# Kernel tuning notes

Measured on AMD Instinct MI355X. Metric: run time of the kernel, lower is better.

The kernel has to match this reference:

```python
import jax, jax.numpy as jnp
import numpy as np

KS = 3      # kernel size
PAD = 1     # zero padding
STRIDE = 1
N = KS * KS # 9 sampling points per pixel


def _deform_conv(feature, offset, weight):
    """DeformConv2d: bilinear sample at learned offsets then 3x3 conv (no bias)."""
    b, c, h, w = feature.shape
    x = jnp.pad(feature, ((0, 0), (0, 0), (PAD, PAD), (PAD, PAD)))
    hp, wp = h + 2 * PAD, w + 2 * PAD
    dt = feature.dtype
    # p_n: kernel grid offsets, x(rows) first then y(cols) -> (2N,)
    rng = jnp.arange(-(KS - 1) // 2, (KS - 1) // 2 + 1, dtype=dt)
    pn_x, pn_y = jnp.meshgrid(rng, rng, indexing='ij')
    # p_0: base sampling grid starting at 1 (accounts for zero padding)
    p0_x, p0_y = jnp.meshgrid(jnp.arange(1, h + 1, dtype=dt),
                              jnp.arange(1, w + 1, dtype=dt), indexing='ij')
    # sampling locations p = p_0 + p_n + offset, split into x/y -> (b,h,w,N)
    off = jnp.transpose(offset, (0, 2, 3, 1))  # (b,h,w,2N)
    px = p0_x[None, :, :, None] + pn_x.reshape(-1)[None, None, None, :] + off[..., :N]
    py = p0_y[None, :, :, None] + pn_y.reshape(-1)[None, None, None, :] + off[..., N:]
    q_lt_x = jnp.clip(jnp.floor(px), 0, hp - 1)
    q_lt_y = jnp.clip(jnp.floor(py), 0, wp - 1)
    q_rb_x = jnp.clip(jnp.floor(px) + 1, 0, hp - 1)
    q_rb_y = jnp.clip(jnp.floor(py) + 1, 0, wp - 1)
    px = jnp.clip(px, 0, hp - 1)
    py = jnp.clip(py, 0, wp - 1)
    # bilinear weights for the 4 corners
    g_lt = (1 + (q_lt_x - px)) * (1 + (q_lt_y - py))
    g_rb = (1 - (q_rb_x - px)) * (1 - (q_rb_y - py))
    g_lb = (1 + (q_lt_x - px)) * (1 - (q_rb_y - py))
    g_rt = (1 - (q_rb_x - px)) * (1 + (q_lt_y - py))
    x_flat = x.reshape(b, c, hp * wp)

    def gather(qx, qy):
        idx = (qx * wp + qy).astype(jnp.int32).reshape(b, 1, -1)
        v = jnp.take_along_axis(x_flat, jnp.broadcast_to(idx, (b, c, h * w * N)), axis=2)
        return v.reshape(b, c, h, w, N)

    x_off = (g_lt[:, None] * gather(q_lt_x, q_lt_y)
             + g_rb[:, None] * gather(q_rb_x, q_rb_y)
             + g_lb[:, None] * gather(q_lt_x, q_rb_y)
             + g_rt[:, None] * gather(q_rb_x, q_lt_y))  # (b,c,h,w,N)
    # equivalent of _reshape_x_offset + conv(ks, stride=ks)
    x_off = x_off.reshape(b, c, h, w, KS, KS)
    return jnp.einsum('bchwij,ocij->bohw', x_off, weight)


def setup_inputs() -> dict:
    key = jax.random.key(0)
    k1, k2, k3 = jax.random.split(key, 3)
    B, C, H, W = 4, 256, 64, 64
    feature = jax.random.normal(k1, (B, C, H, W), dtype=jnp.float32)
    offset = jax.random.normal(k2, (B, 2 * N, H, W), dtype=jnp.float32)
    weight = jax.random.normal(k3, (C, C, KS, KS), dtype=jnp.float32) / np.sqrt(C * N)
    return {"feature": feature, "offset": offset, "weight": weight}


def reference(feature, offset, weight):
    f1 = jax.nn.relu(_deform_conv(feature, offset, weight))
    return jax.nn.relu(f1 + feature)
```

## Files before the change

### kernel.cpp

```cpp
#include <hip/hip_runtime.h>

#define HW    4096
#define J_TOT 16384
#define K_TOT 2304
#define C_CH  256

typedef unsigned short u16;
typedef unsigned int   u32;
typedef __attribute__((ext_vector_type(8))) short short8;
typedef __attribute__((ext_vector_type(4))) float f32x4;
typedef __attribute__((ext_vector_type(4))) unsigned short us4;

__device__ __forceinline__ float b2f(u16 u) { return __uint_as_float(((u32)u) << 16); }
__device__ __forceinline__ u16 f2b(float x) {
  u32 u = __float_as_uint(x);
  u += 0x7FFFu + ((u >> 16) & 1u);
  return (u16)(u >> 16);
}

__device__ __forceinline__ void gload_lds16(const u16* g, u16* l) {
  __builtin_amdgcn_global_load_lds(
      (__attribute__((address_space(1))) void*)(void*)g,
      (__attribute__((address_space(3))) void*)(void*)l, 16, 0, 0);
}

__global__ void k_detect(const u16* __restrict__ f, int* __restrict__ flag) {
  __shared__ int sh[256];
  int t = threadIdx.x;
  int hits = 0;
  for (int i = t; i < 2048; i += 256) {
    u16 u = f[2 * i];
    int e = (u >> 7) & 0xFF;
    hits += (e >= 100 && e <= 141) ? 1 : 0;
  }
  sh[t] = hits;
  __syncthreads();
  if (t == 0) {
    int s = 0;
    for (int i = 0; i < 256; i++) s += sh[i];
    flag[0] = (s > 1024) ? 1 : 0;
  }
}

__global__ void k_prep(const void* __restrict__ featv, u16* __restrict__ ftr,
                       const void* __restrict__ wv, u16* __restrict__ Wr,
                       const int* __restrict__ flag) {
  int isbf = *flag;
  int tx = threadIdx.x;
  int ty = threadIdx.y;
  int z = blockIdx.z;
  if (z < 4) {
    __shared__ u16 tile[32][33];
    int b = z;
    int hw0 = blockIdx.x << 5;
    int c0 = blockIdx.y << 5;
    if (isbf) {
      const u16* f = (const u16*)featv;
#pragma unroll
      for (int i = 0; i < 4; i++) {
        int c = c0 + ty + i * 8;
        tile[ty + i * 8][tx] = f[(((size_t)(b * C_CH + c)) << 12) + hw0 + tx];
      }
    } else {
      const float* f = (const float*)featv;
#pragma unroll
      for (int i = 0; i < 4; i++) {
        int c = c0 + ty + i * 8;
        tile[ty + i * 8][tx] = f2b(f[(((size_t)(b * C_CH + c)) << 12) + hw0 + tx]);
      }
    }
    __syncthreads();
#pragma unroll
    for (int i = 0; i < 4; i++) {
      int hw = hw0 + ty + i * 8;
      ftr[(((size_t)(b * HW + hw)) << 8) + c0 + tx] = tile[tx][ty + i * 8];
    }
  } else {
    int bid = blockIdx.x + (blockIdx.y << 7);
    int flat = ty * 32 + tx;
    for (int idx = bid * 256 + flat; idx < C_CH * K_TOT; idx += 1024 * 256) {
      int c = idx & 255;
      int n = (idx >> 8) % 9;
      int o = idx / K_TOT;
      int src = (o * 256 + c) * 9 + n;
      if (isbf) Wr[idx] = ((const u16*)wv)[src];
      else      Wr[idx] = f2b(((const float*)wv)[src]);
    }
  }
}

#define NT 36

#define A_DMA(Ab)                                                            \
  do {                                                                       \
    gload_lds16(asrc0, (Ab) + wave * 1024);                                  \
    gload_lds16(asrc1, (Ab) + wave * 1024 + 512);                            \
    asrc0 += 64; asrc1 += 64;                                                \
  } while (0)

#define PLOAD_S(tile, P)                                                     \
  do {                                                                       \
    if (((tile) & 3) == 0) {                                                 \
      int np_ = (tile) >> 2;                                                 \
      tw0 = gs[np_][0][pp]; tw1 = gs[np_][1][pp];                            \
      tw2 = gs[np_][2][pp]; tw3 = gs[np_][3][pp];                            \
      ti0 = isx[np_][0][pp]; ti1 = isx[np_][1][pp];                          \
      ti2 = isx[np_][2][pp]; ti3 = isx[np_][3][pp];                          \
    }                                                                        \
    int c0_ = (((tile) & 3) << 6) + cb4;                                     \
    P##w0 = tw0; P##w1 = tw1; P##w2 = tw2; P##w3 = tw3;                      \
    P##q0 = *(const us4*)(ftr + ti0 + c0_);                                  \
    P##q1 = *(const us4*)(ftr + ti1 + c0_);                                  \
    P##q2 = *(const us4*)(ftr + ti2 + c0_);                                  \
    P##q3 = *(const us4*)(ftr + ti3 + c0_);                                  \
  } while (0)

#define PFIN_S(P, Bb)                                                        \
  do {                                                                       \
    us4 ov;                                                                  \
    _Pragma("unroll")                                                        \
    for (int i = 0; i < 4; i++) {                                            \
      float v = P##w0 * b2f(P##q0[i]) + P##w1 * b2f(P##q1[i]) +              \
                P##w2 * b2f(P##q2[i]) + P##w3 * b2f(P##q3[i]);               \
      ov[i] = f2b(v);                                                        \
    }                                                                        \
    *(us4*)((Bb) + bofs) = ov;                                               \
  } while (0)

#define GEMM_COMPUTE(Ab, Bb)                                                 \
  do {                                                                       \
    short8 af[2][2], bf[2][2];                                               \
    _Pragma("unroll")                                                        \
    for (int kk = 0; kk < 2; kk++) {                                         \
      int go = (((kk << 2) + lk) ^ swz) << 3;                                \
      _Pragma("unroll")                                                      \
      for (int oi = 0; oi < 2; oi++)                                         \
        af[oi][kk] = *(const short8*)((Ab) + (wo * 32 + oi * 16 + lr) * 64 + go); \
      _Pragma("unroll")                                                      \
      for (int ji = 0; ji < 2; ji++)                                         \
        bf[ji][kk] = *(const short8*)((Bb) + (wj * 32 + ji * 16 + lr) * 64 + go); \
    }                                                                        \
    __builtin_amdgcn_s_setprio(1);                                           \
    _Pragma("unroll")                                                        \
    for (int kk = 0; kk < 2; kk++)                                           \
      _Pragma("unroll")                                                      \
      for (int oi = 0; oi < 2; oi++)                                         \
        _Pragma("unroll")                                                    \
        for (int ji = 0; ji < 2; ji++)                                       \
          acc[oi][ji] = __builtin_amdgcn_mfma_f32_16x16x32_bf16(             \
              af[oi][kk], bf[ji][kk], acc[oi][ji], 0, 0, 0);                 \
    __builtin_amdgcn_s_setprio(0);                                           \
  } while (0)

#define CBAR()                                                               \
  do {                                                                       \
    asm volatile("s_waitcnt vmcnt(6) lgkmcnt(0)" ::: "memory");              \
    __builtin_amdgcn_s_barrier();                                            \
  } while (0)

#define ROTATE()                                                             \
  do {                                                                       \
    u16* tp_ = Ac; Ac = An; An = Af; Af = tp_;                               \
    tp_ = Bc; Bc = Bn; Bn = Bf; Bf = tp_;                                    \
  } while (0)

__global__ __launch_bounds__(1024, 4) void k_gemm(const u16* __restrict__ Wr,
                                                  const u16* __restrict__ ftr,
                                                  const void* __restrict__ offv,
                                                  const void* __restrict__ featv,
                                                  void* __restrict__ outv,
                                                  const int* __restrict__ flag) {
  __shared__ u16 As[3][256 * 64];
  __shared__ u16 Bs[3][64 * 64];
  __shared__ float gs[9][4][64];
  __shared__ int   isx[9][4][64];
  int isbf = *flag;
  asm volatile("" :: "s"(isbf));
  int j0 = blockIdx.x << 6;
  int b = j0 >> 12;
  int hw0 = j0 & (HW - 1);
  int t = threadIdx.x;
  int wave = t >> 6, lane = t & 63;
  int wj = wave >> 3, wo = wave & 7;
  int lr = lane & 15, lk = lane >> 4;
  int swz = lr & 7;

  if (t < 576) {
    int n = t >> 6, p = t & 63;
    int hw = hw0 + p;
    int h = hw >> 6, w = hw & 63;
    size_t obi = (((size_t)(b * 18 + n)) << 12) + hw;
    float ox, oy;
    if (isbf) {
      const u16* po = (const u16*)offv;
      ox = b2f(po[obi]);
      oy = b2f(po[obi + (9u << 12)]);
    } else {
      const float* po = (const float*)offv;
      ox = po[obi];
      oy = po[obi + (9u << 12)];
    }
    int ki = n / 3, kj = n % 3;
    float px = (float)(h + ki) + ox;
    float py = (float)(w + kj) + oy;
    float fx = floorf(px), fy = floorf(py);
    float qltx = fminf(fmaxf(fx, 0.f), 65.f);
    float qlty = fminf(fmaxf(fy, 0.f), 65.f);
    float qrbx = fminf(fmaxf(fx + 1.f, 0.f), 65.f);
    float qrby = fminf(fmaxf(fy + 1.f, 0.f), 65.f);
    float pcx = fminf(fmaxf(px, 0.f), 65.f);
    float pcy = fminf(fmaxf(py, 0.f), 65.f);
    float dltx = 1.f + (qltx - pcx);
    float drbx = 1.f - (qrbx - pcx);
    float dlty = 1.f + (qlty - pcy);
    float drby = 1.f - (qrby - pcy);
    float g0 = dltx * dlty;
    float g1 = drbx * drby;
    float g2 = dltx * drby;
    float g3 = drbx * dlty;
    int x0 = (int)qltx, y0 = (int)qlty, x1 = (int)qrbx, y1 = (int)qrby;
    int v0 = (x0 >= 1 && x0 <= 64 && y0 >= 1 && y0 <= 64);
    int v1 = (x1 >= 1 && x1 <= 64 && y1 >= 1 && y1 <= 64);
    int v2 = (x0 >= 1 && x0 <= 64 && y1 >= 1 && y1 <= 64);
    int v3 = (x1 >= 1 && x1 <= 64 && y0 >= 1 && y0 <= 64);
    int base = b << 12;
    isx[n][0][p] = v0 ? ((base + ((x0 - 1) << 6) + (y0 - 1)) << 8) : 0;
    isx[n][1][p] = v1 ? ((base + ((x1 - 1) << 6) + (y1 - 1)) << 8) : 0;
    isx[n][2][p] = v2 ? ((base + ((x0 - 1) << 6) + (y1 - 1)) << 8) : 0;
    isx[n][3][p] = v3 ? ((base + ((x1 - 1) << 6) + (y0 - 1)) << 8) : 0;
    gs[n][0][p] = v0 ? g0 : 0.f;
    gs[n][1][p] = v1 ? g1 : 0.f;
    gs[n][2][p] = v2 ? g2 : 0.f;
    gs[n][3][p] = v3 ? g3 : 0.f;
  }

  f32x4 acc[2][2];
  f32x4 zero = {0.f, 0.f, 0.f, 0.f};
#pragma unroll
  for (int i = 0; i < 2; i++)
#pragma unroll
    for (int j = 0; j < 2; j++) acc[i][j] = zero;

  int rb = lane >> 3;
  int cs = ((lane & 7) ^ rb) << 3;
  const u16* asrc0 = Wr + (size_t)(wave * 16 + 0 + rb) * K_TOT + cs;
  const u16* asrc1 = Wr + (size_t)(wave * 16 + 8 + rb) * K_TOT + cs;

  int pp = t >> 4, qq = t & 15;
  int cgp = qq >> 1, half = qq & 1;
  int bofs = pp * 64 + ((cgp ^ (pp & 7)) << 3) + (half << 2);
  int cb4 = (cgp << 3) + (half << 2);

  u16 *Ac = &As[0][0], *An = &As[1][0], *Af = &As[2][0];
  u16 *Bc = &Bs[0][0], *Bn = &Bs[1][0], *Bf = &Bs[2][0];

  __syncthreads();

  us4 aq0, aq1, aq2, aq3, bq0, bq1, bq2, bq3;
  float aw0, aw1, aw2, aw3, bw0, bw1, bw2, bw3;
  float tw0, tw1, tw2, tw3;
  int ti0, ti1, ti2, ti3;

  PLOAD_S(0, a); A_DMA(Ac);
  PFIN_S(a, Bc);
  PLOAD_S(1, b); A_DMA(An);
  CBAR();

#pragma unroll 1
  for (int it = 0; it < 17; ++it) {
    PLOAD_S(2 * it + 2, a);
    A_DMA(Af);
    GEMM_COMPUTE(Ac, Bc);
    PFIN_S(b, Bn);
    CBAR();
    ROTATE();
    PLOAD_S(2 * it + 3, b);
    A_DMA(Af);
    GEMM_COMPUTE(Ac, Bc);
    PFIN_S(a, Bn);
    CBAR();
    ROTATE();
  }
  GEMM_COMPUTE(Ac, Bc);
  PFIN_S(b, Bn);
  asm volatile("s_waitcnt vmcnt(0) lgkmcnt(0)" ::: "memory");
  __builtin_amdgcn_s_barrier();
  GEMM_COMPUTE(An, Bn);

  int lq = lane >> 4;
#pragma unroll
  for (int oi = 0; oi < 2; oi++) {
#pragma unroll
    for (int ji = 0; ji < 2; ji++) {
      int j = j0 + wj * 32 + ji * 16 + lr;
      int bb_ = j >> 12, hw = j & (HW - 1);
      int o0 = wo * 32 + oi * 16 + lq * 4;
#pragma unroll
      for (int r = 0; r < 4; r++) {
        size_t oidx = (((size_t)(bb_ * C_CH + o0 + r)) << 12) + hw;
        float v = acc[oi][ji][r];
        v = fmaxf(v, 0.f);
        float ft = isbf ? b2f(((const u16*)featv)[oidx]) : ((const float*)featv)[oidx];
        v = fmaxf(v + ft, 0.f);
        if (isbf) ((u16*)outv)[oidx] = f2b(v);
        else      ((float*)outv)[oidx] = v;
      }
    }
  }
}

extern "C" void kernel_launch(void* const* d_in, const int* in_sizes, int n_in,
                              void* d_out, int out_size, void* d_ws, size_t ws_size,
                              hipStream_t stream) {
  const void* feat = d_in[0];
  const void* offs = d_in[1];
  const void* wght = d_in[2];

  const size_t off_flag = 0;
  const size_t off_wr   = 256;
  const size_t off_ftr  = off_wr + (size_t)1179648;
  const size_t need     = off_ftr + (size_t)8388608;
  if (ws_size < need) return;

  char* ws = (char*)d_ws;
  int* flag = (int*)(ws + off_flag);
  u16* Wr   = (u16*)(ws + off_wr);
  u16* ftr  = (u16*)(ws + off_ftr);

  k_detect<<<1, 256, 0, stream>>>((const u16*)feat, flag);
  k_prep<<<dim3(128, 8, 5), dim3(32, 8), 0, stream>>>(feat, ftr, wght, Wr, flag);
  k_gemm<<<J_TOT / 64, 1024, 0, stream>>>(Wr, ftr, offs, feat, d_out, flag);
}
```

Before: 128.0 us.

## Load weight fragments directly to registers and halve GEMM block tile

Replaces the LDS-staged DMA of weight tiles with direct global-to-register loads of MFMA fragments, prefetched one K-step ahead. Blocks shrink to 512 threads covering 32 pixel columns, doubling the grid, and block IDs are remapped to spread neighbouring tiles across dies. This frees LDS and barrier pressure but doubles weight reads from L2 and relies on compiler-inserted waits for global latency.

```diff
diff --git a/kernel.cpp b/kernel.cpp
--- a/kernel.cpp
+++ b/kernel.cpp
@@ -16,12 +16,6 @@
   u32 u = __float_as_uint(x);
   u += 0x7FFFu + ((u >> 16) & 1u);
   return (u16)(u >> 16);
-}
-
-__device__ __forceinline__ void gload_lds16(const u16* g, u16* l) {
-  __builtin_amdgcn_global_load_lds(
-      (__attribute__((address_space(1))) void*)(void*)g,
-      (__attribute__((address_space(3))) void*)(void*)l, 16, 0, 0);
 }
 
 __global__ void k_detect(const u16* __restrict__ f, int* __restrict__ flag) {
@@ -91,11 +85,15 @@
 
 #define NT 36
 
-#define A_DMA(Ab)                                                            \
-  do {                                                                       \
-    gload_lds16(asrc0, (Ab) + wave * 1024);                                  \
-    gload_lds16(asrc1, (Ab) + wave * 1024 + 512);                            \
-    asrc0 += 64; asrc1 += 64;                                                \
+#define MFMA_ __builtin_amdgcn_mfma_f32_16x16x32_bf16
+
+#define ALOAD(tile, P)                                                       \
+  do {                                                                       \
+    const u16* ab_ = Wr + awoff + (tile) * 64;                               \
+    P##00 = *(const short8*)(ab_);                                           \
+    P##01 = *(const short8*)(ab_ + 32);                                      \
+    P##10 = *(const short8*)(ab_ + 16 * K_TOT);                              \
+    P##11 = *(const short8*)(ab_ + 16 * K_TOT + 32);                         \
   } while (0)
 
 #define PLOAD_S(tile, P)                                                     \
@@ -127,66 +125,60 @@
     *(us4*)((Bb) + bofs) = ov;                                               \
   } while (0)
 
-#define GEMM_COMPUTE(Ab, Bb)                                                 \
-  do {                                                                       \
-    short8 af[2][2], bf[2][2];                                               \
-    _Pragma("unroll")                                                        \
-    for (int kk = 0; kk < 2; kk++) {                                         \
-      int go = (((kk << 2) + lk) ^ swz) << 3;                                \
-      _Pragma("unroll")                                                      \
-      for (int oi = 0; oi < 2; oi++)                                         \
-        af[oi][kk] = *(const short8*)((Ab) + (wo * 32 + oi * 16 + lr) * 64 + go); \
-      _Pragma("unroll")                                                      \
-      for (int ji = 0; ji < 2; ji++)                                         \
-        bf[ji][kk] = *(const short8*)((Bb) + (wj * 32 + ji * 16 + lr) * 64 + go); \
-    }                                                                        \
+#define GEMM_COMPUTE(P, Bb)                                                  \
+  do {                                                                       \
+    int go0 = (lk ^ swz) << 3;                                               \
+    int go1 = ((4 + lk) ^ swz) << 3;                                         \
+    short8 b00 = *(const short8*)((Bb) + lr * 64 + go0);                     \
+    short8 b10 = *(const short8*)((Bb) + (16 + lr) * 64 + go0);              \
+    short8 b01 = *(const short8*)((Bb) + lr * 64 + go1);                     \
+    short8 b11 = *(const short8*)((Bb) + (16 + lr) * 64 + go1);              \
     __builtin_amdgcn_s_setprio(1);                                           \
-    _Pragma("unroll")                                                        \
-    for (int kk = 0; kk < 2; kk++)                                           \
-      _Pragma("unroll")                                                      \
-      for (int oi = 0; oi < 2; oi++)                                         \
-        _Pragma("unroll")                                                    \
-        for (int ji = 0; ji < 2; ji++)                                       \
-          acc[oi][ji] = __builtin_amdgcn_mfma_f32_16x16x32_bf16(             \
-              af[oi][kk], bf[ji][kk], acc[oi][ji], 0, 0, 0);                 \
+    acc[0][0] = MFMA_(P##00, b00, acc[0][0], 0, 0, 0);                       \
+    acc[0][1] = MFMA_(P##00, b10, acc[0][1], 0, 0, 0);                       \
+    acc[1][0] = MFMA_(P##10, b00, acc[1][0], 0, 0, 0);                       \
+    acc[1][1] = MFMA_(P##10, b10, acc[1][1], 0, 0, 0);                       \
+    acc[0][0] = MFMA_(P##01, b01, acc[0][0], 0, 0, 0);                       \
+    acc[0][1] = MFMA_(P##01, b11, acc[0][1], 0, 0, 0);                       \
+    acc[1][0] = MFMA_(P##11, b01, acc[1][0], 0, 0, 0);                       \
+    acc[1][1] = MFMA_(P##11, b11, acc[1][1], 0, 0, 0);                       \
     __builtin_amdgcn_s_setprio(0);                                           \
   } while (0)
 
 #define CBAR()                                                               \
   do {                                                                       \
-    asm volatile("s_waitcnt vmcnt(6) lgkmcnt(0)" ::: "memory");              \
+    asm volatile("s_waitcnt lgkmcnt(0)" ::: "memory");                       \
     __builtin_amdgcn_s_barrier();                                            \
   } while (0)
 
 #define ROTATE()                                                             \
   do {                                                                       \
-    u16* tp_ = Ac; Ac = An; An = Af; Af = tp_;                               \
-    tp_ = Bc; Bc = Bn; Bn = Bf; Bf = tp_;                                    \
-  } while (0)
-
-__global__ __launch_bounds__(1024, 4) void k_gemm(const u16* __restrict__ Wr,
-                                                  const u16* __restrict__ ftr,
-                                                  const void* __restrict__ offv,
-                                                  const void* __restrict__ featv,
-                                                  void* __restrict__ outv,
-                                                  const int* __restrict__ flag) {
-  __shared__ u16 As[3][256 * 64];
-  __shared__ u16 Bs[3][64 * 64];
-  __shared__ float gs[9][4][64];
-  __shared__ int   isx[9][4][64];
+    u16* tp_ = Bc; Bc = Bn; Bn = Bf; Bf = tp_;                               \
+  } while (0)
+
+__global__ __launch_bounds__(512, 4) void k_gemm(const u16* __restrict__ Wr,
+                                                 const u16* __restrict__ ftr,
+                                                 const void* __restrict__ offv,
+                                                 const void* __restrict__ featv,
+                                                 void* __restrict__ outv,
+                                                 const int* __restrict__ flag) {
+  __shared__ u16 Bs[3][32 * 64];
+  __shared__ float gs[9][4][32];
+  __shared__ int   isx[9][4][32];
   int isbf = *flag;
-  asm volatile("" :: "s"(isbf));
-  int j0 = blockIdx.x << 6;
+  int bid = blockIdx.x;
+  int xb = (bid & 7) * 64 + (bid >> 3);
+  int j0 = xb << 5;
   int b = j0 >> 12;
   int hw0 = j0 & (HW - 1);
   int t = threadIdx.x;
   int wave = t >> 6, lane = t & 63;
-  int wj = wave >> 3, wo = wave & 7;
+  int wo = wave;
   int lr = lane & 15, lk = lane >> 4;
   int swz = lr & 7;
 
-  if (t < 576) {
-    int n = t >> 6, p = t & 63;
+  if (t < 288) {
+    int n = t >> 5, p = t & 31;
     int hw = hw0 + p;
     int h = hw >> 6, w = hw & 63;
     size_t obi = (((size_t)(b * 18 + n)) << 12) + hw;
@@ -241,17 +233,13 @@
 #pragma unroll
     for (int j = 0; j < 2; j++) acc[i][j] = zero;
 
-  int rb = lane >> 3;
-  int cs = ((lane & 7) ^ rb) << 3;
-  const u16* asrc0 = Wr + (size_t)(wave * 16 + 0 + rb) * K_TOT + cs;
-  const u16* asrc1 = Wr + (size_t)(wave * 16 + 8 + rb) * K_TOT + cs;
+  const size_t awoff = (size_t)(wo * 32 + lr) * K_TOT + lk * 8;
 
   int pp = t >> 4, qq = t & 15;
   int cgp = qq >> 1, half = qq & 1;
   int bofs = pp * 64 + ((cgp ^ (pp & 7)) << 3) + (half << 2);
   int cb4 = (cgp << 3) + (half << 2);
 
-  u16 *Ac = &As[0][0], *An = &As[1][0], *Af = &As[2][0];
   u16 *Bc = &Bs[0][0], *Bn = &Bs[1][0], *Bf = &Bs[2][0];
 
   __syncthreads();
@@ -260,39 +248,41 @@
   float aw0, aw1, aw2, aw3, bw0, bw1, bw2, bw3;
   float tw0, tw1, tw2, tw3;
   int ti0, ti1, ti2, ti3;
-
-  PLOAD_S(0, a); A_DMA(Ac);
+  short8 ua00, ua01, ua10, ua11, ub00, ub01, ub10, ub11;
+
+  ALOAD(0, ua);
+  PLOAD_S(0, a);
   PFIN_S(a, Bc);
-  PLOAD_S(1, b); A_DMA(An);
+  PLOAD_S(1, b);
   CBAR();
 
 #pragma unroll 1
   for (int it = 0; it < 17; ++it) {
+    ALOAD(2 * it + 1, ub);
     PLOAD_S(2 * it + 2, a);
-    A_DMA(Af);
-    GEMM_COMPUTE(Ac, Bc);
+    GEMM_COMPUTE(ua, Bc);
     PFIN_S(b, Bn);
     CBAR();
     ROTATE();
+    ALOAD(2 * it + 2, ua);
     PLOAD_S(2 * it + 3, b);
-    A_DMA(Af);
-    GEMM_COMPUTE(Ac, Bc);
+    GEMM_COMPUTE(ub, Bc);
     PFIN_S(a, Bn);
     CBAR();
     ROTATE();
   }
-  GEMM_COMPUTE(Ac, Bc);
+  ALOAD(35, ub);
+  GEMM_COMPUTE(ua, Bc);
   PFIN_S(b, Bn);
-  asm volatile("s_waitcnt vmcnt(0) lgkmcnt(0)" ::: "memory");
-  __builtin_amdgcn_s_barrier();
-  GEMM_COMPUTE(An, Bn);
+  CBAR();
+  GEMM_COMPUTE(ub, Bn);
 
   int lq = lane >> 4;
 #pragma unroll
   for (int oi = 0; oi < 2; oi++) {
 #pragma unroll
     for (int ji = 0; ji < 2; ji++) {
-      int j = j0 + wj * 32 + ji * 16 + lr;
+      int j = j0 + ji * 16 + lr;
       int bb_ = j >> 12, hw = j & (HW - 1);
       int o0 = wo * 32 + oi * 16 + lq * 4;
 #pragma unroll
@@ -329,5 +319,5 @@
 
   k_detect<<<1, 256, 0, stream>>>((const u16*)feat, flag);
   k_prep<<<dim3(128, 8, 5), dim3(32, 8), 0, stream>>>(feat, ftr, wght, Wr, flag);
-  k_gemm<<<J_TOT / 64, 1024, 0, stream>>>(Wr, ftr, offs, feat, d_out, flag);
-}
+  k_gemm<<<J_TOT / 32, 512, 0, stream>>>(Wr, ftr, offs, feat, d_out, flag);
+}
```

New measurement: 167.0 us. 30.5% more time.
